# Optimization experiments

Measured on AMD Instinct MI355X. Metric: run time of the kernel, lower is better.

The kernel has to match this reference:

```python
import jax, jax.numpy as jnp
import numpy as np
from functools import partial

N_NODES = 50000
BN_EPS = 1e-5


def _renumber(src, dst, mask, n_nodes):
    # Faithful to extract_batch_edge_idx: kept edges are relabeled by the rank of
    # their node id among the sorted unique node ids APPEARING in kept edges.
    m = mask.astype(jnp.int32)
    appear = jnp.zeros(n_nodes, jnp.int32)
    appear = appear.at[src].max(m)
    appear = appear.at[dst].max(m)
    new_id = jnp.cumsum(appear) - 1  # rank of each appearing node id
    s = jnp.where(mask, new_id[src], 0)
    d = jnp.where(mask, new_id[dst], 0)
    return s, d


def _gcn_conv(x, W, b, src, dst, ew, n):
    # PyG GCNConv: linear, add self-loops, symmetric normalization, scatter-add.
    xw = x @ W                                   # [n, out]
    deg = jax.ops.segment_sum(ew, dst, num_segments=n) + 1.0  # +1 self loop
    dinv = jax.lax.rsqrt(deg)
    norm = dinv[src] * dinv[dst] * ew            # masked edges -> 0 weight
    agg = jax.ops.segment_sum(norm[:, None] * xw[src], dst, num_segments=n)
    agg = agg + (dinv * dinv)[:, None] * xw      # self-loop contribution
    return agg + b


def setup_inputs() -> dict:
    key = jax.random.key(0)
    ks = jax.random.split(key, 8)
    R, N, E, B = 3, N_NODES, 1000000, 2048
    inp, hid, out = 256, 512, 256
    features = jax.random.normal(ks[0], (R, N, inp), jnp.float32)
    W1 = jax.random.normal(ks[1], (inp, hid), jnp.float32) * (1.0 / np.sqrt(inp))
    b1 = jnp.zeros((hid,), jnp.float32)
    W2 = jax.random.normal(ks[2], (hid, out), jnp.float32) * (1.0 / np.sqrt(hid))
    b2 = jnp.zeros((out,), jnp.float32)
    gamma = jnp.ones((hid,), jnp.float32)
    beta = jnp.zeros((hid,), jnp.float32)
    edge_index = jax.random.randint(ks[3], (R, 2, E), 0, N, jnp.int64)
    # distinct, sorted batch node ids (torch code iterates node values)
    batch_nodes = jnp.sort(jax.random.permutation(ks[4], N)[:B]).astype(jnp.int64)
    return {"features": features, "W1": W1, "b1": b1, "W2": W2, "b2": b2,
            "gamma": gamma, "beta": beta, "edge_index": edge_index,
            "batch_nodes": batch_nodes}


def reference(features, W1, b1, W2, b2, gamma, beta, edge_index, batch_nodes):
    R, N, _ = features.shape
    B = batch_nodes.shape[0]
    in_batch = jnp.zeros(N, bool).at[batch_nodes].set(True)
    outs = []
    for r in range(R):  # small fixed relation count
        src, dst = edge_index[r, 0], edge_index[r, 1]
        mask = in_batch[src] & in_batch[dst]
        ew = mask.astype(features.dtype)
        s, d = _renumber(src, dst, mask, N)
        x = features[r, batch_nodes]             # [B, inp]
        h = _gcn_conv(x, W1, b1, s, d, ew, B)    # [B, hid]
        # BatchNorm1d (training mode: biased batch stats)
        mu = h.mean(axis=0)
        var = h.var(axis=0)
        h = (h - mu) * jax.lax.rsqrt(var + BN_EPS) * gamma + beta
        outs.append(_gcn_conv(h, W2, b2, s, d, ew, B))  # [B, out]
    stacked = jnp.stack(outs, axis=0)            # [R, B, out]
    return stacked.reshape(B, -1)                # row-major reshape, as torch
```

## Files before the change

### kernel.cpp

```cpp
#include <hip/hip_runtime.h>
#include <hip/hip_bf16.h>
#include <stdint.h>
#include <stddef.h>

#define RNUM   3
#define NNODES 50000
#define ENUM   1000000
#define BATCH  2048
#define INP    256
#define HID    512
#define OUTC   256
#define BN_EPS 1e-5f

typedef __bf16 bf16x8 __attribute__((ext_vector_type(8)));
typedef float  f32x4  __attribute__((ext_vector_type(4)));

__device__ inline unsigned short f2bf(float f) {
    union { float f; unsigned u; } c; c.f = f;
    unsigned u = c.u;
    return (unsigned short)((u + 0x7fffu + ((u >> 16) & 1u)) >> 16);
}

__device__ inline uint4 pack8(float4 a, float4 b) {
    uint4 r;
    r.x = (unsigned)f2bf(a.x) | ((unsigned)f2bf(a.y) << 16);
    r.y = (unsigned)f2bf(a.z) | ((unsigned)f2bf(a.w) << 16);
    r.z = (unsigned)f2bf(b.x) | ((unsigned)f2bf(b.y) << 16);
    r.w = (unsigned)f2bf(b.z) | ((unsigned)f2bf(b.w) << 16);
    return r;
}

__global__ __launch_bounds__(256) void k_wt(const float* __restrict__ W1,
                                            const float* __restrict__ W2,
                                            unsigned short* __restrict__ W1T,
                                            unsigned short* __restrict__ W2T) {
    __shared__ float T[32][33];
    int z = blockIdx.z;
    const float* W = z ? W2 : W1;
    unsigned short* WT = z ? W2T : W1T;
    int K = z ? HID : INP;
    int N = z ? OUTC : HID;
    int kt = blockIdx.y, nt = blockIdx.x;
    if (kt * 32 >= K || nt * 32 >= N) return;
    int tx = threadIdx.x & 31, ty = threadIdx.x >> 5;
#pragma unroll
    for (int j = 0; j < 4; ++j)
        T[ty + j * 8][tx] = W[(size_t)(kt * 32 + ty + j * 8) * N + nt * 32 + tx];
    __syncthreads();
#pragma unroll
    for (int j = 0; j < 4; ++j)
        WT[(size_t)(nt * 32 + ty + j * 8) * K + kt * 32 + tx] = f2bf(T[tx][ty + j * 8]);
}

__global__ void k_init(int* __restrict__ inv, int* __restrict__ appear,
                       float* __restrict__ deg, float* __restrict__ musum,
                       float* __restrict__ sqsum, int* __restrict__ kcount) {
    int i = blockIdx.x * blockDim.x + threadIdx.x;
    if (i < NNODES) inv[i] = -1;
    if (i < RNUM * BATCH) { appear[i] = 0; deg[i] = 0.0f; }
    if (i < RNUM * HID)   { musum[i] = 0.0f; sqsum[i] = 0.0f; }
    if (i < RNUM)         kcount[i] = 0;
}

__global__ void k_scatter_inv(const int* __restrict__ bn, int* __restrict__ inv) {
    int i = blockIdx.x * blockDim.x + threadIdx.x;
    if (i < BATCH) inv[bn[i]] = i;
}

__global__ void k_mask(const int* __restrict__ edge_index, const int* __restrict__ inv,
                       int* __restrict__ appear, int2* __restrict__ edges,
                       int* __restrict__ kcount) {
    int z = blockIdx.z;
    const int* src = edge_index + (size_t)z * 2 * ENUM;
    const int* dst = src + ENUM;
    int2* ed = edges + (size_t)z * ENUM;
    int* app = appear + z * BATCH;
    int stride = gridDim.x * blockDim.x;
    for (int e4 = blockIdx.x * blockDim.x + threadIdx.x; e4 < ENUM / 4; e4 += stride) {
        int4 s4 = ((const int4*)src)[e4];
        int4 d4 = ((const int4*)dst)[e4];
        int ss[4] = {s4.x, s4.y, s4.z, s4.w};
        int dd[4] = {d4.x, d4.y, d4.z, d4.w};
#pragma unroll
        for (int i = 0; i < 4; ++i) {
            int ps = inv[ss[i]];
            int pd = inv[dd[i]];
            if (ps >= 0 && pd >= 0) {
                int idx = atomicAdd(kcount + z, 1);
                ed[idx] = make_int2(ps, pd);
                app[ps] = 1;
                app[pd] = 1;
            }
        }
    }
}

__global__ __launch_bounds__(1024) void k_scan2048(const int* __restrict__ appear,
                                                   int* __restrict__ rankArr) {
    __shared__ int buf[2][BATCH];
    int z = blockIdx.x;
    const int* ap = appear + z * BATCH;
    int* rk = rankArr + z * BATCH;
    int t = threadIdx.x;
    buf[0][t] = ap[t];
    buf[0][t + 1024] = ap[t + 1024];
    __syncthreads();
    int cur = 0;
    for (int off = 1; off < BATCH; off <<= 1) {
        int nxt = cur ^ 1;
        int i1 = t, i2 = t + 1024;
        buf[nxt][i1] = buf[cur][i1] + (i1 >= off ? buf[cur][i1 - off] : 0);
        buf[nxt][i2] = buf[cur][i2] + (i2 >= off ? buf[cur][i2 - off] : 0);
        __syncthreads();
        cur = nxt;
    }
    rk[t] = buf[cur][t] - 1;
    rk[t + 1024] = buf[cur][t + 1024] - 1;
}

__global__ void k_deg(int2* __restrict__ edges, const int* __restrict__ rankArr,
                      const int* __restrict__ kcount, float* __restrict__ deg) {
    int z = blockIdx.z;
    int K = kcount[z];
    int2* ed = edges + (size_t)z * ENUM;
    const int* rk = rankArr + z * BATCH;
    float* dg = deg + z * BATCH;
    int stride = gridDim.x * blockDim.x;
    for (int e = blockIdx.x * blockDim.x + threadIdx.x; e < K; e += stride) {
        int2 E = ed[e];
        int s = rk[E.x], d = rk[E.y];
        ed[e] = make_int2(s, d);
        atomicAdd(&dg[d], 1.0f);
    }
}


__global__ __launch_bounds__(256) void k_gemm1(
    const float* __restrict__ features, const int* __restrict__ bn,
    const unsigned short* __restrict__ W1T, const float* __restrict__ b1,
    const float* __restrict__ deg, float* __restrict__ xw, float* __restrict__ hbase) {
    __shared__ __align__(16) unsigned short As[64][40];
    __shared__ __align__(16) unsigned short Bs[64][40];
    int z = blockIdx.z;
    const float* feat = features + (size_t)z * NNODES * INP;
    const float* dgz = deg + z * BATCH;
    float* xwz = xw + (size_t)z * BATCH * HID;
    float* hbz = hbase + (size_t)z * BATCH * HID;
    int m0 = blockIdx.y * 64, n0 = blockIdx.x * 64;
    int t = threadIdx.x;
    int ar = t >> 2, aq = t & 3;
    int grow = bn[m0 + ar];
    const float* aptr = feat + (size_t)grow * INP + aq * 8;
    const unsigned short* bptr = W1T + (size_t)(n0 + ar) * INP + aq * 8;

    int lane = t & 63, wave = t >> 6;
    int wm = (wave & 1) * 32, wn = (wave >> 1) * 32;
    int ml = lane & 15, quad = lane >> 4, q8 = quad * 8;

    f32x4 acc[2][2] = {};
    for (int k0 = 0; k0 < INP; k0 += 32) {
        float4 a0 = *(const float4*)(aptr + k0);
        float4 a1 = *(const float4*)(aptr + k0 + 4);
        uint4 bv = *(const uint4*)(bptr + k0);
        *(uint4*)&As[ar][aq * 8] = pack8(a0, a1);
        *(uint4*)&Bs[ar][aq * 8] = bv;
        __syncthreads();
        bf16x8 af[2], bfr[2];
#pragma unroll
        for (int mi = 0; mi < 2; ++mi) af[mi]  = *(const bf16x8*)&As[wm + mi * 16 + ml][q8];
#pragma unroll
        for (int ni = 0; ni < 2; ++ni) bfr[ni] = *(const bf16x8*)&Bs[wn + ni * 16 + ml][q8];
#pragma unroll
        for (int mi = 0; mi < 2; ++mi)
#pragma unroll
            for (int ni = 0; ni < 2; ++ni)
                acc[mi][ni] = __builtin_amdgcn_mfma_f32_16x16x32_bf16(af[mi], bfr[ni], acc[mi][ni], 0, 0, 0);
        __syncthreads();
    }
#pragma unroll
    for (int mi = 0; mi < 2; ++mi)
#pragma unroll
        for (int r = 0; r < 4; ++r) {
            int row = m0 + wm + mi * 16 + quad * 4 + r;
            float d2 = 1.0f / (dgz[row] + 1.0f);
#pragma unroll
            for (int ni = 0; ni < 2; ++ni) {
                int col = n0 + wn + ni * 16 + ml;
                float c = acc[mi][ni][r];
                xwz[(size_t)row * HID + col] = c;
                hbz[(size_t)row * HID + col] = d2 * c + b1[col];
            }
        }
}

__global__ __launch_bounds__(256) void k_gemm2(
    const float* __restrict__ hbase, const float* __restrict__ rstdg,
    const float* __restrict__ shiftc, const unsigned short* __restrict__ W2T,
    const float* __restrict__ b2, const float* __restrict__ deg,
    float* __restrict__ yw, float* __restrict__ out) {
    __shared__ __align__(16) unsigned short As[64][40];
    __shared__ __align__(16) unsigned short Bs[64][40];
    int z = blockIdx.z;
    const float* hz = hbase + (size_t)z * BATCH * HID;
    const float* gz = rstdg + z * HID;
    const float* sz = shiftc + z * HID;
    const float* dgz = deg + z * BATCH;
    float* ywz = yw + (size_t)z * BATCH * OUTC;
    float* oz = out + (size_t)z * BATCH * OUTC;
    int m0 = blockIdx.y * 64, n0 = blockIdx.x * 64;
    int t = threadIdx.x;
    int ar = t >> 2, aq = t & 3;
    const float* aptr = hz + (size_t)(m0 + ar) * HID + aq * 8;
    const unsigned short* bptr = W2T + (size_t)(n0 + ar) * HID + aq * 8;

    int lane = t & 63, wave = t >> 6;
    int wm = (wave & 1) * 32, wn = (wave >> 1) * 32;
    int ml = lane & 15, quad = lane >> 4, q8 = quad * 8;

    f32x4 acc[2][2] = {};
    for (int k0 = 0; k0 < HID; k0 += 32) {
        float4 h0 = *(const float4*)(aptr + k0);
        float4 h1 = *(const float4*)(aptr + k0 + 4);
        float4 g0 = *(const float4*)(gz + k0 + aq * 8);
        float4 g1 = *(const float4*)(gz + k0 + aq * 8 + 4);
        float4 s0 = *(const float4*)(sz + k0 + aq * 8);
        float4 s1 = *(const float4*)(sz + k0 + aq * 8 + 4);
        float4 a0 = make_float4(h0.x * g0.x + s0.x, h0.y * g0.y + s0.y,
                                h0.z * g0.z + s0.z, h0.w * g0.w + s0.w);
        float4 a1 = make_float4(h1.x * g1.x + s1.x, h1.y * g1.y + s1.y,
                                h1.z * g1.z + s1.z, h1.w * g1.w + s1.w);
        uint4 bv = *(const uint4*)(bptr + k0);
        *(uint4*)&As[ar][aq * 8] = pack8(a0, a1);
        *(uint4*)&Bs[ar][aq * 8] = bv;
        __syncthreads();
        bf16x8 af[2], bfr[2];
#pragma unroll
        for (int mi = 0; mi < 2; ++mi) af[mi]  = *(const bf16x8*)&As[wm + mi * 16 + ml][q8];
#pragma unroll
        for (int ni = 0; ni < 2; ++ni) bfr[ni] = *(const bf16x8*)&Bs[wn + ni * 16 + ml][q8];
#pragma unroll
        for (int mi = 0; mi < 2; ++mi)
#pragma unroll
            for (int ni = 0; ni < 2; ++ni)
                acc[mi][ni] = __builtin_amdgcn_mfma_f32_16x16x32_bf16(af[mi], bfr[ni], acc[mi][ni], 0, 0, 0);
        __syncthreads();
    }
#pragma unroll
    for (int mi = 0; mi < 2; ++mi)
#pragma unroll
        for (int r = 0; r < 4; ++r) {
            int row = m0 + wm + mi * 16 + quad * 4 + r;
            float d2 = 1.0f / (dgz[row] + 1.0f);
#pragma unroll
            for (int ni = 0; ni < 2; ++ni) {
                int col = n0 + wn + ni * 16 + ml;
                float c = acc[mi][ni][r];
                ywz[(size_t)row * OUTC + col] = c;
                oz[(size_t)row * OUTC + col] = d2 * c + b2[col];
            }
        }
}

__global__ void k_agg(const int2* __restrict__ edges, const int* __restrict__ kcount,
                      const float* __restrict__ deg, const float* __restrict__ src_mat,
                      float* __restrict__ dst_mat, int ncol) {
    int z = blockIdx.z;
    int K = kcount[z];
    const int2* ed = edges + (size_t)z * ENUM;
    const float* dgz = deg + z * BATCH;
    const float* sm = src_mat + (size_t)z * BATCH * ncol;
    float* dm = dst_mat + (size_t)z * BATCH * ncol;
    for (int e = blockIdx.x; e < K; e += gridDim.x) {
        int2 E = ed[e];
        float w = rsqrtf(dgz[E.x] + 1.0f) * rsqrtf(dgz[E.y] + 1.0f);
        const float* srow = sm + (size_t)E.x * ncol;
        float* drow = dm + (size_t)E.y * ncol;
        for (int c = threadIdx.x; c < ncol; c += blockDim.x)
            atomicAdd(&drow[c], w * srow[c]);
    }
}

__global__ __launch_bounds__(256) void k_bnstats(const float* __restrict__ hbase,
                                                 float* __restrict__ musum,
                                                 float* __restrict__ sqsum) {
    int z = blockIdx.z;
    const float* h = hbase + (size_t)z * BATCH * HID;
    int c0 = threadIdx.x;
    int r0 = blockIdx.x * 32;
    float s1a = 0, s2a = 0, s1b = 0, s2b = 0;
    for (int rr = 0; rr < 32; ++rr) {
        const float* row = h + (size_t)(r0 + rr) * HID;
        float va = row[c0];
        float vb = row[c0 + 256];
        s1a += va; s2a += va * va;
        s1b += vb; s2b += vb * vb;
    }
    atomicAdd(&musum[z * HID + c0], s1a);       atomicAdd(&sqsum[z * HID + c0], s2a);
    atomicAdd(&musum[z * HID + c0 + 256], s1b); atomicAdd(&sqsum[z * HID + c0 + 256], s2b);
}

__global__ void k_bnfinal(const float* __restrict__ musum, const float* __restrict__ sqsum,
                          const float* __restrict__ gamma, const float* __restrict__ beta,
                          float* __restrict__ rstdg, float* __restrict__ shiftc) {
    int z = blockIdx.x;
    int c = threadIdx.x;
    float mu = musum[z * HID + c] * (1.0f / BATCH);
    float ex2 = sqsum[z * HID + c] * (1.0f / BATCH);
    float var = ex2 - mu * mu;
    float g = rsqrtf(var + BN_EPS) * gamma[c];
    rstdg[z * HID + c] = g;
    shiftc[z * HID + c] = beta[c] - mu * g;
}

extern "C" void kernel_launch(void* const* d_in, const int* in_sizes, int n_in,
                              void* d_out, int out_size, void* d_ws, size_t ws_size,
                              hipStream_t stream) {
    const float* features    = (const float*)d_in[0];
    const float* W1          = (const float*)d_in[1];
    const float* b1          = (const float*)d_in[2];
    const float* W2          = (const float*)d_in[3];
    const float* b2          = (const float*)d_in[4];
    const float* gamma       = (const float*)d_in[5];
    const float* beta        = (const float*)d_in[6];
    const int*   edge_index  = (const int*)d_in[7];
    const int*   batch_nodes = (const int*)d_in[8];
    float* out = (float*)d_out;

    char* p = (char*)d_ws;
    size_t cur = 0;
    auto alloc = [&](size_t bytes) {
        void* r = p + cur;
        cur = (cur + bytes + 255) & ~(size_t)255;
        return r;
    };
    int*   inv    = (int*)  alloc(NNODES * sizeof(int));
    int*   appear = (int*)  alloc(RNUM * BATCH * sizeof(int));
    int*   rankA  = (int*)  alloc(RNUM * BATCH * sizeof(int));
    int*   kcount = (int*)  alloc(RNUM * sizeof(int));
    float* deg    = (float*)alloc(RNUM * BATCH * sizeof(float));
    float* musum  = (float*)alloc(RNUM * HID * sizeof(float));
    float* sqsum  = (float*)alloc(RNUM * HID * sizeof(float));
    float* rstdg  = (float*)alloc(RNUM * HID * sizeof(float));
    float* shiftc = (float*)alloc(RNUM * HID * sizeof(float));
    unsigned short* W1T = (unsigned short*)alloc((size_t)HID * INP * sizeof(unsigned short));
    unsigned short* W2T = (unsigned short*)alloc((size_t)OUTC * HID * sizeof(unsigned short));
    int2*  edges  = (int2*) alloc((size_t)RNUM * ENUM * sizeof(int2));
    float* xw     = (float*)alloc((size_t)RNUM * BATCH * HID * sizeof(float));
    float* hbase  = (float*)alloc((size_t)RNUM * BATCH * HID * sizeof(float));
    float* yw     = (float*)alloc((size_t)RNUM * BATCH * OUTC * sizeof(float));
    (void)ws_size; (void)in_sizes; (void)n_in; (void)out_size;

    k_wt<<<dim3(16, 16, 2), 256, 0, stream>>>(W1, W2, W1T, W2T);
    k_init<<<(NNODES + 255) / 256, 256, 0, stream>>>(inv, appear, deg, musum, sqsum, kcount);
    k_scatter_inv<<<BATCH / 256, 256, 0, stream>>>(batch_nodes, inv);

    k_mask<<<dim3(512, 1, RNUM), 256, 0, stream>>>(edge_index, inv, appear, edges, kcount);
    k_scan2048<<<RNUM, 1024, 0, stream>>>(appear, rankA);
    k_deg<<<dim3(64, 1, RNUM), 256, 0, stream>>>(edges, rankA, kcount, deg);

    k_gemm1<<<dim3(HID / 64, BATCH / 64, RNUM), 256, 0, stream>>>(
        features, batch_nodes, W1T, b1, deg, xw, hbase);
    k_agg<<<dim3(256, 1, RNUM), 256, 0, stream>>>(edges, kcount, deg, xw, hbase, HID);

    k_bnstats<<<dim3(64, 1, RNUM), 256, 0, stream>>>(hbase, musum, sqsum);
    k_bnfinal<<<RNUM, HID, 0, stream>>>(musum, sqsum, gamma, beta, rstdg, shiftc);

    k_gemm2<<<dim3(OUTC / 64, BATCH / 64, RNUM), 256, 0, stream>>>(
        hbase, rstdg, shiftc, W2T, b2, deg, yw, out);
    k_agg<<<dim3(256, 1, RNUM), 256, 0, stream>>>(edges, kcount, deg, yw, out, OUTC);
}
```

Before: 328.1 us.

## Fuse setup, mask+GEMM1, scan+degree and BN-finalize into fewer kernel launches

Merges the init, weight-transpose and bf16 feature gather into one setup kernel, and fuses edge masking (now a shared-memory bitmap membership test) with the first GEMM in a single grid. It also replaces the 2048-wide scan and degree kernels with one wave-shuffle scan plus shared-memory degree accumulation per relation. The BN finalize step is folded into GEMM2, and the h computation moves into the BN stats kernel via a separate aggregation buffer. This cuts the launch count and the repeated fp32 feature conversion. In exchange it adds an extra buffer pass and serializes each relation's degree counting within a single block.

After: 322.6 us, median of 2. No clear change (-1.7%).

```diff
diff --git a/kernel.cpp b/kernel.cpp
--- a/kernel.cpp
+++ b/kernel.cpp
@@ -11,6 +11,9 @@
 #define HID    512
 #define OUTC   256
 #define BN_EPS 1e-5f
+#define NBLK   768
+#define NTHR   256
+#define BMW    1568
 
 typedef __bf16 bf16x8 __attribute__((ext_vector_type(8)));
 typedef float  f32x4  __attribute__((ext_vector_type(4)));
@@ -30,235 +33,200 @@
     return r;
 }
 
-__global__ __launch_bounds__(256) void k_wt(const float* __restrict__ W1,
-                                            const float* __restrict__ W2,
-                                            unsigned short* __restrict__ W1T,
-                                            unsigned short* __restrict__ W2T) {
-    __shared__ float T[32][33];
-    int z = blockIdx.z;
-    const float* W = z ? W2 : W1;
-    unsigned short* WT = z ? W2T : W1T;
-    int K = z ? HID : INP;
-    int N = z ? OUTC : HID;
-    int kt = blockIdx.y, nt = blockIdx.x;
-    if (kt * 32 >= K || nt * 32 >= N) return;
-    int tx = threadIdx.x & 31, ty = threadIdx.x >> 5;
-#pragma unroll
-    for (int j = 0; j < 4; ++j)
-        T[ty + j * 8][tx] = W[(size_t)(kt * 32 + ty + j * 8) * N + nt * 32 + tx];
-    __syncthreads();
-#pragma unroll
-    for (int j = 0; j < 4; ++j)
-        WT[(size_t)(nt * 32 + ty + j * 8) * K + kt * 32 + tx] = f2bf(T[tx][ty + j * 8]);
-}
-
-__global__ void k_init(int* __restrict__ inv, int* __restrict__ appear,
-                       float* __restrict__ deg, float* __restrict__ musum,
-                       float* __restrict__ sqsum, int* __restrict__ kcount) {
-    int i = blockIdx.x * blockDim.x + threadIdx.x;
-    if (i < NNODES) inv[i] = -1;
-    if (i < RNUM * BATCH) { appear[i] = 0; deg[i] = 0.0f; }
-    if (i < RNUM * HID)   { musum[i] = 0.0f; sqsum[i] = 0.0f; }
-    if (i < RNUM)         kcount[i] = 0;
-}
-
-__global__ void k_scatter_inv(const int* __restrict__ bn, int* __restrict__ inv) {
-    int i = blockIdx.x * blockDim.x + threadIdx.x;
-    if (i < BATCH) inv[bn[i]] = i;
-}
-
-__global__ void k_mask(const int* __restrict__ edge_index, const int* __restrict__ inv,
-                       int* __restrict__ appear, int2* __restrict__ edges,
-                       int* __restrict__ kcount) {
-    int z = blockIdx.z;
-    const int* src = edge_index + (size_t)z * 2 * ENUM;
-    const int* dst = src + ENUM;
-    int2* ed = edges + (size_t)z * ENUM;
-    int* app = appear + z * BATCH;
-    int stride = gridDim.x * blockDim.x;
-    for (int e4 = blockIdx.x * blockDim.x + threadIdx.x; e4 < ENUM / 4; e4 += stride) {
-        int4 s4 = ((const int4*)src)[e4];
-        int4 d4 = ((const int4*)dst)[e4];
-        int ss[4] = {s4.x, s4.y, s4.z, s4.w};
-        int dd[4] = {d4.x, d4.y, d4.z, d4.w};
-#pragma unroll
-        for (int i = 0; i < 4; ++i) {
-            int ps = inv[ss[i]];
-            int pd = inv[dd[i]];
-            if (ps >= 0 && pd >= 0) {
-                int idx = atomicAdd(kcount + z, 1);
-                ed[idx] = make_int2(ps, pd);
-                app[ps] = 1;
-                app[pd] = 1;
+__global__ __launch_bounds__(256) void k_setup(
+    const float* __restrict__ features, const float* __restrict__ W1,
+    const float* __restrict__ W2, const int* __restrict__ bn,
+    unsigned* __restrict__ bitmap, int* __restrict__ inv,
+    int* __restrict__ appear, int* __restrict__ kcount,
+    float* __restrict__ musum, float* __restrict__ sqsum,
+    float* __restrict__ aggbuf,
+    unsigned short* __restrict__ W1T, unsigned short* __restrict__ W2T,
+    unsigned short* __restrict__ featB) {
+    __shared__ float T[32 * 33];
+    const int tid = threadIdx.x;
+    const int bid = blockIdx.x;
+
+    {
+        float4* a4 = (float4*)aggbuf;
+        int base = bid * 1024;
+#pragma unroll
+        for (int j = 0; j < 4; ++j)
+            a4[base + j * 256 + tid] = make_float4(0.f, 0.f, 0.f, 0.f);
+    }
+
+    if (bid == 0) {
+        for (int i = tid; i < BMW; i += NTHR) bitmap[i] = 0u;
+        __syncthreads();
+        for (int i = tid; i < BATCH; i += NTHR) {
+            int v = bn[i];
+            atomicOr(&bitmap[v >> 5], 1u << (v & 31));
+        }
+    } else if (bid == 1) {
+        for (int i = tid; i < BATCH; i += NTHR) inv[bn[i]] = i;
+        for (int i = tid; i < RNUM * BATCH; i += NTHR) appear[i] = 0;
+        for (int i = tid; i < RNUM * HID; i += NTHR) { musum[i] = 0.f; sqsum[i] = 0.f; }
+        if (tid < RNUM) kcount[tid] = 0;
+    }
+
+    if (bid < 256) {
+        int i = bid;
+        int z = i >> 7; i &= 127;
+        const float* W = z ? W2 : W1;
+        unsigned short* WT = z ? W2T : W1T;
+        int K = z ? HID : INP;
+        int N = z ? OUTC : HID;
+        int kt, nt;
+        if (z == 0) { nt = i & 15; kt = i >> 4; } else { nt = i & 7; kt = i >> 3; }
+        int tx = tid & 31, ty = tid >> 5;
+#pragma unroll
+        for (int j = 0; j < 4; ++j)
+            T[(ty + j * 8) * 33 + tx] = W[(size_t)(kt * 32 + ty + j * 8) * N + nt * 32 + tx];
+        __syncthreads();
+#pragma unroll
+        for (int j = 0; j < 4; ++j)
+            WT[(size_t)(nt * 32 + ty + j * 8) * K + kt * 32 + tx] = f2bf(T[tx * 33 + ty + j * 8]);
+    } else if (bid < 640) {
+        int i = bid - 256;
+        int row = i * 16 + (tid >> 4);
+        int c0 = (tid & 15) * 16;
+        int z = row >> 11, m = row & 2047;
+        const float* srow = features + ((size_t)z * NNODES + bn[m]) * INP;
+        unsigned short* drow = featB + (size_t)row * INP;
+        float4 f0 = *(const float4*)(srow + c0);
+        float4 f1 = *(const float4*)(srow + c0 + 4);
+        float4 f2 = *(const float4*)(srow + c0 + 8);
+        float4 f3 = *(const float4*)(srow + c0 + 12);
+        *(uint4*)(drow + c0)     = pack8(f0, f1);
+        *(uint4*)(drow + c0 + 8) = pack8(f2, f3);
+    }
+}
+
+__global__ __launch_bounds__(256) void k_maskgemm1(
+    const int* __restrict__ edge_index, const unsigned* __restrict__ bitmap,
+    const int* __restrict__ inv, int* __restrict__ appear,
+    int* __restrict__ kcount, int2* __restrict__ edges,
+    const unsigned short* __restrict__ featB,
+    const unsigned short* __restrict__ W1T, float* __restrict__ xw) {
+    __shared__ __align__(16) unsigned char smem[10240];
+    const int tid = threadIdx.x;
+    const int bid = blockIdx.x;
+
+    {
+        unsigned* bmL = (unsigned*)smem;
+        for (int i = tid; i < BMW; i += NTHR) bmL[i] = bitmap[i];
+        __syncthreads();
+        const int gsz = NBLK * NTHR;
+        const int g0 = bid * NTHR + tid;
+        for (int z = 0; z < RNUM; ++z) {
+            const int4* s4 = (const int4*)(edge_index + (size_t)z * 2 * ENUM);
+            const int4* d4 = (const int4*)(edge_index + (size_t)z * 2 * ENUM + ENUM);
+            int2* ed = edges + (size_t)z * ENUM;
+            int* app = appear + z * BATCH;
+            for (int i = g0; i < ENUM / 4; i += gsz) {
+                int4 S = s4[i], D = d4[i];
+                int ss[4] = {S.x, S.y, S.z, S.w};
+                int dd[4] = {D.x, D.y, D.z, D.w};
+#pragma unroll
+                for (int u = 0; u < 4; ++u) {
+                    int s = ss[u], d = dd[u];
+                    unsigned ks = (bmL[s >> 5] >> (s & 31)) & 1u;
+                    unsigned kd = (bmL[d >> 5] >> (d & 31)) & 1u;
+                    if (ks & kd) {
+                        int ps = inv[s], pd = inv[d];
+                        int idx = atomicAdd(&kcount[z], 1);
+                        ed[idx] = make_int2(ps, pd);
+                        app[ps] = 1;
+                        app[pd] = 1;
+                    }
+                }
             }
         }
-    }
-}
-
-__global__ __launch_bounds__(1024) void k_scan2048(const int* __restrict__ appear,
-                                                   int* __restrict__ rankArr) {
-    __shared__ int buf[2][BATCH];
-    int z = blockIdx.x;
+        __syncthreads();
+    }
+
+    {
+        unsigned short* As = (unsigned short*)smem;
+        unsigned short* Bs = (unsigned short*)(smem + 5120);
+        int z = bid >> 8;
+        int r = bid & 255;
+        int n0 = (r & 7) * 64, m0 = (r >> 3) * 64;
+        int ar = tid >> 2, aq = tid & 3;
+        const unsigned short* aptr = featB + (size_t)(z * BATCH + m0 + ar) * INP + aq * 8;
+        const unsigned short* bptr = W1T + (size_t)(n0 + ar) * INP + aq * 8;
+        int lane = tid & 63, wave = tid >> 6;
+        int wm = (wave & 1) * 32, wn = (wave >> 1) * 32;
+        int ml = lane & 15, quad = lane >> 4, q8 = quad * 8;
+        f32x4 acc[2][2] = {};
+        for (int k0 = 0; k0 < INP; k0 += 32) {
+            uint4 av = *(const uint4*)(aptr + k0);
+            uint4 bv = *(const uint4*)(bptr + k0);
+            *(uint4*)&As[ar * 40 + aq * 8] = av;
+            *(uint4*)&Bs[ar * 40 + aq * 8] = bv;
+            __syncthreads();
+            bf16x8 af[2], bfr[2];
+#pragma unroll
+            for (int mi = 0; mi < 2; ++mi) af[mi]  = *(const bf16x8*)&As[(wm + mi * 16 + ml) * 40 + q8];
+#pragma unroll
+            for (int ni = 0; ni < 2; ++ni) bfr[ni] = *(const bf16x8*)&Bs[(wn + ni * 16 + ml) * 40 + q8];
+#pragma unroll
+            for (int mi = 0; mi < 2; ++mi)
+#pragma unroll
+                for (int ni = 0; ni < 2; ++ni)
+                    acc[mi][ni] = __builtin_amdgcn_mfma_f32_16x16x32_bf16(af[mi], bfr[ni], acc[mi][ni], 0, 0, 0);
+            __syncthreads();
+        }
+        float* xwz = xw + (size_t)z * BATCH * HID;
+#pragma unroll
+        for (int mi = 0; mi < 2; ++mi)
+#pragma unroll
+            for (int rr = 0; rr < 4; ++rr) {
+                int row = m0 + wm + mi * 16 + quad * 4 + rr;
+#pragma unroll
+                for (int ni = 0; ni < 2; ++ni) {
+                    int col = n0 + wn + ni * 16 + ml;
+                    xwz[(size_t)row * HID + col] = acc[mi][ni][rr];
+                }
+            }
+    }
+}
+
+__global__ __launch_bounds__(256) void k_scandeg(
+    const int* __restrict__ appear, const int* __restrict__ kcount,
+    int2* __restrict__ edges, float* __restrict__ deg) {
+    __shared__ int rk[BATCH];
+    __shared__ float dgf[BATCH];
+    __shared__ int wsums[4];
+    const int tid = threadIdx.x;
+    const int z = blockIdx.x;
     const int* ap = appear + z * BATCH;
-    int* rk = rankArr + z * BATCH;
-    int t = threadIdx.x;
-    buf[0][t] = ap[t];
-    buf[0][t + 1024] = ap[t + 1024];
+    int b0 = tid * 8;
+    int pre[8]; int run = 0;
+#pragma unroll
+    for (int j = 0; j < 8; ++j) { run += ap[b0 + j]; pre[j] = run; }
+    int lane = tid & 63, wv = tid >> 6;
+    int sc = run;
+    for (int off = 1; off < 64; off <<= 1) {
+        int n = __shfl_up(sc, off);
+        if (lane >= off) sc += n;
+    }
+    if (lane == 63) wsums[wv] = sc;
     __syncthreads();
-    int cur = 0;
-    for (int off = 1; off < BATCH; off <<= 1) {
-        int nxt = cur ^ 1;
-        int i1 = t, i2 = t + 1024;
-        buf[nxt][i1] = buf[cur][i1] + (i1 >= off ? buf[cur][i1 - off] : 0);
-        buf[nxt][i2] = buf[cur][i2] + (i2 >= off ? buf[cur][i2 - off] : 0);
-        __syncthreads();
-        cur = nxt;
-    }
-    rk[t] = buf[cur][t] - 1;
-    rk[t + 1024] = buf[cur][t + 1024] - 1;
-}
-
-__global__ void k_deg(int2* __restrict__ edges, const int* __restrict__ rankArr,
-                      const int* __restrict__ kcount, float* __restrict__ deg) {
-    int z = blockIdx.z;
+    int base = sc - run;
+    for (int w = 0; w < wv; ++w) base += wsums[w];
+#pragma unroll
+    for (int j = 0; j < 8; ++j) { rk[b0 + j] = base + pre[j] - 1; dgf[b0 + j] = 0.f; }
+    __syncthreads();
     int K = kcount[z];
     int2* ed = edges + (size_t)z * ENUM;
-    const int* rk = rankArr + z * BATCH;
-    float* dg = deg + z * BATCH;
-    int stride = gridDim.x * blockDim.x;
-    for (int e = blockIdx.x * blockDim.x + threadIdx.x; e < K; e += stride) {
+    for (int e = tid; e < K; e += NTHR) {
         int2 E = ed[e];
         int s = rk[E.x], d = rk[E.y];
         ed[e] = make_int2(s, d);
-        atomicAdd(&dg[d], 1.0f);
-    }
-}
-
-
-__global__ __launch_bounds__(256) void k_gemm1(
-    const float* __restrict__ features, const int* __restrict__ bn,
-    const unsigned short* __restrict__ W1T, const float* __restrict__ b1,
-    const float* __restrict__ deg, float* __restrict__ xw, float* __restrict__ hbase) {
-    __shared__ __align__(16) unsigned short As[64][40];
-    __shared__ __align__(16) unsigned short Bs[64][40];
-    int z = blockIdx.z;
-    const float* feat = features + (size_t)z * NNODES * INP;
-    const float* dgz = deg + z * BATCH;
-    float* xwz = xw + (size_t)z * BATCH * HID;
-    float* hbz = hbase + (size_t)z * BATCH * HID;
-    int m0 = blockIdx.y * 64, n0 = blockIdx.x * 64;
-    int t = threadIdx.x;
-    int ar = t >> 2, aq = t & 3;
-    int grow = bn[m0 + ar];
-    const float* aptr = feat + (size_t)grow * INP + aq * 8;
-    const unsigned short* bptr = W1T + (size_t)(n0 + ar) * INP + aq * 8;
-
-    int lane = t & 63, wave = t >> 6;
-    int wm = (wave & 1) * 32, wn = (wave >> 1) * 32;
-    int ml = lane & 15, quad = lane >> 4, q8 = quad * 8;
-
-    f32x4 acc[2][2] = {};
-    for (int k0 = 0; k0 < INP; k0 += 32) {
-        float4 a0 = *(const float4*)(aptr + k0);
-        float4 a1 = *(const float4*)(aptr + k0 + 4);
-        uint4 bv = *(const uint4*)(bptr + k0);
-        *(uint4*)&As[ar][aq * 8] = pack8(a0, a1);
-        *(uint4*)&Bs[ar][aq * 8] = bv;
-        __syncthreads();
-        bf16x8 af[2], bfr[2];
-#pragma unroll
-        for (int mi = 0; mi < 2; ++mi) af[mi]  = *(const bf16x8*)&As[wm + mi * 16 + ml][q8];
-#pragma unroll
-        for (int ni = 0; ni < 2; ++ni) bfr[ni] = *(const bf16x8*)&Bs[wn + ni * 16 + ml][q8];
-#pragma unroll
-        for (int mi = 0; mi < 2; ++mi)
-#pragma unroll
-            for (int ni = 0; ni < 2; ++ni)
-                acc[mi][ni] = __builtin_amdgcn_mfma_f32_16x16x32_bf16(af[mi], bfr[ni], acc[mi][ni], 0, 0, 0);
-        __syncthreads();
-    }
-#pragma unroll
-    for (int mi = 0; mi < 2; ++mi)
-#pragma unroll
-        for (int r = 0; r < 4; ++r) {
-            int row = m0 + wm + mi * 16 + quad * 4 + r;
-            float d2 = 1.0f / (dgz[row] + 1.0f);
-#pragma unroll
-            for (int ni = 0; ni < 2; ++ni) {
-                int col = n0 + wn + ni * 16 + ml;
-                float c = acc[mi][ni][r];
-                xwz[(size_t)row * HID + col] = c;
-                hbz[(size_t)row * HID + col] = d2 * c + b1[col];
-            }
-        }
-}
-
-__global__ __launch_bounds__(256) void k_gemm2(
-    const float* __restrict__ hbase, const float* __restrict__ rstdg,
-    const float* __restrict__ shiftc, const unsigned short* __restrict__ W2T,
-    const float* __restrict__ b2, const float* __restrict__ deg,
-    float* __restrict__ yw, float* __restrict__ out) {
-    __shared__ __align__(16) unsigned short As[64][40];
-    __shared__ __align__(16) unsigned short Bs[64][40];
-    int z = blockIdx.z;
-    const float* hz = hbase + (size_t)z * BATCH * HID;
-    const float* gz = rstdg + z * HID;
-    const float* sz = shiftc + z * HID;
-    const float* dgz = deg + z * BATCH;
-    float* ywz = yw + (size_t)z * BATCH * OUTC;
-    float* oz = out + (size_t)z * BATCH * OUTC;
-    int m0 = blockIdx.y * 64, n0 = blockIdx.x * 64;
-    int t = threadIdx.x;
-    int ar = t >> 2, aq = t & 3;
-    const float* aptr = hz + (size_t)(m0 + ar) * HID + aq * 8;
-    const unsigned short* bptr = W2T + (size_t)(n0 + ar) * HID + aq * 8;
-
-    int lane = t & 63, wave = t >> 6;
-    int wm = (wave & 1) * 32, wn = (wave >> 1) * 32;
-    int ml = lane & 15, quad = lane >> 4, q8 = quad * 8;
-
-    f32x4 acc[2][2] = {};
-    for (int k0 = 0; k0 < HID; k0 += 32) {
-        float4 h0 = *(const float4*)(aptr + k0);
-        float4 h1 = *(const float4*)(aptr + k0 + 4);
-        float4 g0 = *(const float4*)(gz + k0 + aq * 8);
-        float4 g1 = *(const float4*)(gz + k0 + aq * 8 + 4);
-        float4 s0 = *(const float4*)(sz + k0 + aq * 8);
-        float4 s1 = *(const float4*)(sz + k0 + aq * 8 + 4);
-        float4 a0 = make_float4(h0.x * g0.x + s0.x, h0.y * g0.y + s0.y,
-                                h0.z * g0.z + s0.z, h0.w * g0.w + s0.w);
-        float4 a1 = make_float4(h1.x * g1.x + s1.x, h1.y * g1.y + s1.y,
-                                h1.z * g1.z + s1.z, h1.w * g1.w + s1.w);
-        uint4 bv = *(const uint4*)(bptr + k0);
-        *(uint4*)&As[ar][aq * 8] = pack8(a0, a1);
-        *(uint4*)&Bs[ar][aq * 8] = bv;
-        __syncthreads();
-        bf16x8 af[2], bfr[2];
-#pragma unroll
-        for (int mi = 0; mi < 2; ++mi) af[mi]  = *(const bf16x8*)&As[wm + mi * 16 + ml][q8];
-#pragma unroll
-        for (int ni = 0; ni < 2; ++ni) bfr[ni] = *(const bf16x8*)&Bs[wn + ni * 16 + ml][q8];
-#pragma unroll
-        for (int mi = 0; mi < 2; ++mi)
-#pragma unroll
-            for (int ni = 0; ni < 2; ++ni)
-                acc[mi][ni] = __builtin_amdgcn_mfma_f32_16x16x32_bf16(af[mi], bfr[ni], acc[mi][ni], 0, 0, 0);
-        __syncthreads();
-    }
-#pragma unroll
-    for (int mi = 0; mi < 2; ++mi)
-#pragma unroll
-        for (int r = 0; r < 4; ++r) {
-            int row = m0 + wm + mi * 16 + quad * 4 + r;
-            float d2 = 1.0f / (dgz[row] + 1.0f);
-#pragma unroll
-            for (int ni = 0; ni < 2; ++ni) {
-                int col = n0 + wn + ni * 16 + ml;
-                float c = acc[mi][ni][r];
-                ywz[(size_t)row * OUTC + col] = c;
-                oz[(size_t)row * OUTC + col] = d2 * c + b2[col];
-            }
-        }
+        atomicAdd(&dgf[d], 1.0f);
+    }
+    __syncthreads();
+    float* dz = deg + z * BATCH;
+    for (int i = tid; i < BATCH; i += NTHR) dz[i] = dgf[i];
 }
 
 __global__ void k_agg(const int2* __restrict__ edges, const int* __restrict__ kcount,
@@ -280,36 +248,108 @@
     }
 }
 
-__global__ __launch_bounds__(256) void k_bnstats(const float* __restrict__ hbase,
-                                                 float* __restrict__ musum,
-                                                 float* __restrict__ sqsum) {
+__global__ __launch_bounds__(256) void k_hbn(
+    const float* __restrict__ xw, const float* __restrict__ aggbuf,
+    const float* __restrict__ deg, const float* __restrict__ b1,
+    float* __restrict__ hbase, float* __restrict__ musum,
+    float* __restrict__ sqsum) {
     int z = blockIdx.z;
-    const float* h = hbase + (size_t)z * BATCH * HID;
+    const float* xz = xw + (size_t)z * BATCH * HID;
+    const float* az = aggbuf + (size_t)z * BATCH * HID;
+    float* hz = hbase + (size_t)z * BATCH * HID;
+    const float* dgz = deg + z * BATCH;
     int c0 = threadIdx.x;
     int r0 = blockIdx.x * 32;
+    float b1a = b1[c0], b1b = b1[c0 + 256];
     float s1a = 0, s2a = 0, s1b = 0, s2b = 0;
     for (int rr = 0; rr < 32; ++rr) {
-        const float* row = h + (size_t)(r0 + rr) * HID;
-        float va = row[c0];
-        float vb = row[c0 + 256];
-        s1a += va; s2a += va * va;
-        s1b += vb; s2b += vb * vb;
+        int row = r0 + rr;
+        float d2 = 1.0f / (dgz[row] + 1.0f);
+        size_t off = (size_t)row * HID + c0;
+        float ha = xz[off] * d2 + b1a + az[off];
+        float hb = xz[off + 256] * d2 + b1b + az[off + 256];
+        hz[off] = ha;
+        hz[off + 256] = hb;
+        s1a += ha; s2a += ha * ha;
+        s1b += hb; s2b += hb * hb;
     }
     atomicAdd(&musum[z * HID + c0], s1a);       atomicAdd(&sqsum[z * HID + c0], s2a);
     atomicAdd(&musum[z * HID + c0 + 256], s1b); atomicAdd(&sqsum[z * HID + c0 + 256], s2b);
 }
 
-__global__ void k_bnfinal(const float* __restrict__ musum, const float* __restrict__ sqsum,
-                          const float* __restrict__ gamma, const float* __restrict__ beta,
-                          float* __restrict__ rstdg, float* __restrict__ shiftc) {
-    int z = blockIdx.x;
-    int c = threadIdx.x;
-    float mu = musum[z * HID + c] * (1.0f / BATCH);
-    float ex2 = sqsum[z * HID + c] * (1.0f / BATCH);
-    float var = ex2 - mu * mu;
-    float g = rsqrtf(var + BN_EPS) * gamma[c];
-    rstdg[z * HID + c] = g;
-    shiftc[z * HID + c] = beta[c] - mu * g;
+__global__ __launch_bounds__(256) void k_gemm2f(
+    const float* __restrict__ hbase, const float* __restrict__ musum,
+    const float* __restrict__ sqsum, const float* __restrict__ gamma,
+    const float* __restrict__ beta, const unsigned short* __restrict__ W2T,
+    const float* __restrict__ b2, const float* __restrict__ deg,
+    float* __restrict__ yw, float* __restrict__ out) {
+    __shared__ __align__(16) unsigned short As[64][40];
+    __shared__ __align__(16) unsigned short Bs[64][40];
+    __shared__ float gL[HID];
+    __shared__ float sL[HID];
+    int z = blockIdx.z;
+    int m0 = blockIdx.y * 64, n0 = blockIdx.x * 64;
+    int tid = threadIdx.x;
+    for (int c = tid; c < HID; c += NTHR) {
+        float mu  = musum[z * HID + c] * (1.0f / BATCH);
+        float ex2 = sqsum[z * HID + c] * (1.0f / BATCH);
+        float var = ex2 - mu * mu;
+        float g = rsqrtf(var + BN_EPS) * gamma[c];
+        gL[c] = g;
+        sL[c] = beta[c] - mu * g;
+    }
+    __syncthreads();
+    int ar = tid >> 2, aq = tid & 3;
+    const float* aptr = hbase + (size_t)z * BATCH * HID + (size_t)(m0 + ar) * HID + aq * 8;
+    const unsigned short* bptr = W2T + (size_t)(n0 + ar) * HID + aq * 8;
+    int lane = tid & 63, wave = tid >> 6;
+    int wm = (wave & 1) * 32, wn = (wave >> 1) * 32;
+    int ml = lane & 15, quad = lane >> 4, q8 = quad * 8;
+    f32x4 acc[2][2] = {};
+    for (int k0 = 0; k0 < HID; k0 += 32) {
+        float4 h0 = *(const float4*)(aptr + k0);
+        float4 h1 = *(const float4*)(aptr + k0 + 4);
+        float4 g0 = *(const float4*)(gL + k0 + aq * 8);
+        float4 g1 = *(const float4*)(gL + k0 + aq * 8 + 4);
+        float4 s0 = *(const float4*)(sL + k0 + aq * 8);
+        float4 s1 = *(const float4*)(sL + k0 + aq * 8 + 4);
+        float4 a0 = make_float4(h0.x * g0.x + s0.x, h0.y * g0.y + s0.y,
+                                h0.z * g0.z + s0.z, h0.w * g0.w + s0.w);
+        float4 a1 = make_float4(h1.x * g1.x + s1.x, h1.y * g1.y + s1.y,
+                                h1.z * g1.z + s1.z, h1.w * g1.w + s1.w);
+        uint4 bv = *(const uint4*)(bptr + k0);
+        *(uint4*)&As[ar][aq * 8] = pack8(a0, a1);
+        *(uint4*)&Bs[ar][aq * 8] = bv;
+        __syncthreads();
+        bf16x8 af[2], bfr[2];
+#pragma unroll
+        for (int mi = 0; mi < 2; ++mi) af[mi]  = *(const bf16x8*)&As[wm + mi * 16 + ml][q8];
+#pragma unroll
+        for (int ni = 0; ni < 2; ++ni) bfr[ni] = *(const bf16x8*)&Bs[wn + ni * 16 + ml][q8];
+#pragma unroll
+        for (int mi = 0; mi < 2; ++mi)
+#pragma unroll
+            for (int ni = 0; ni < 2; ++ni)
+                acc[mi][ni] = __builtin_amdgcn_mfma_f32_16x16x32_bf16(af[mi], bfr[ni], acc[mi][ni], 0, 0, 0);
+        __syncthreads();
+    }
+    const float* dgz = deg + z * BATCH;
+    float* ywz = yw + (size_t)z * BATCH * OUTC;
+    float* oz = out + (size_t)z * BATCH * OUTC;
+#pragma unroll
+    for (int mi = 0; mi < 2; ++mi)
+#pragma unroll
+        for (int rr = 0; rr < 4; ++rr) {
+            int row = m0 + wm + mi * 16 + quad * 4 + rr;
+            float d2 = 1.0f / (dgz[row] + 1.0f);
+#pragma unroll
+            for (int ni = 0; ni < 2; ++ni) {
+                int col = n0 + wn + ni * 16 + ml;
+                float c = acc[mi][ni][rr];
+                ywz[(size_t)row * OUTC + col] = c;
+                oz[(size_t)row * OUTC + col] = d2 * c + b2[col];
+            }
+        }
 }
 
 extern "C" void kernel_launch(void* const* d_in, const int* in_sizes, int n_in,
@@ -335,37 +375,37 @@
     };
     int*   inv    = (int*)  alloc(NNODES * sizeof(int));
     int*   appear = (int*)  alloc(RNUM * BATCH * sizeof(int));
-    int*   rankA  = (int*)  alloc(RNUM * BATCH * sizeof(int));
     int*   kcount = (int*)  alloc(RNUM * sizeof(int));
     float* deg    = (float*)alloc(RNUM * BATCH * sizeof(float));
     float* musum  = (float*)alloc(RNUM * HID * sizeof(float));
     float* sqsum  = (float*)alloc(RNUM * HID * sizeof(float));
-    float* rstdg  = (float*)alloc(RNUM * HID * sizeof(float));
-    float* shiftc = (float*)alloc(RNUM * HID * sizeof(float));
+    unsigned* bitmap = (unsigned*)alloc(BMW * sizeof(unsigned));
     unsigned short* W1T = (unsigned short*)alloc((size_t)HID * INP * sizeof(unsigned short));
     unsigned short* W2T = (unsigned short*)alloc((size_t)OUTC * HID * sizeof(unsigned short));
+    unsigned short* featB = (unsigned short*)alloc((size_t)RNUM * BATCH * INP * sizeof(unsigned short));
     int2*  edges  = (int2*) alloc((size_t)RNUM * ENUM * sizeof(int2));
     float* xw     = (float*)alloc((size_t)RNUM * BATCH * HID * sizeof(float));
+    float* aggbuf = (float*)alloc((size_t)RNUM * BATCH * HID * sizeof(float));
     float* hbase  = (float*)alloc((size_t)RNUM * BATCH * HID * sizeof(float));
     float* yw     = (float*)alloc((size_t)RNUM * BATCH * OUTC * sizeof(float));
     (void)ws_size; (void)in_sizes; (void)n_in; (void)out_size;
 
-    k_wt<<<dim3(16, 16, 2), 256, 0, stream>>>(W1, W2, W1T, W2T);
-    k_init<<<(NNODES + 255) / 256, 256, 0, stream>>>(inv, appear, deg, musum, sqsum, kcount);
-    k_scatter_inv<<<BATCH / 256, 256, 0, stream>>>(batch_nodes, inv);
-
-    k_mask<<<dim3(512, 1, RNUM), 256, 0, stream>>>(edge_index, inv, appear, edges, kcount);
-    k_scan2048<<<RNUM, 1024, 0, stream>>>(appear, rankA);
-    k_deg<<<dim3(64, 1, RNUM), 256, 0, stream>>>(edges, rankA, kcount, deg);
-
-    k_gemm1<<<dim3(HID / 64, BATCH / 64, RNUM), 256, 0, stream>>>(
-        features, batch_nodes, W1T, b1, deg, xw, hbase);
-    k_agg<<<dim3(256, 1, RNUM), 256, 0, stream>>>(edges, kcount, deg, xw, hbase, HID);
-
-    k_bnstats<<<dim3(64, 1, RNUM), 256, 0, stream>>>(hbase, musum, sqsum);
-    k_bnfinal<<<RNUM, HID, 0, stream>>>(musum, sqsum, gamma, beta, rstdg, shiftc);
-
-    k_gemm2<<<dim3(OUTC / 64, BATCH / 64, RNUM), 256, 0, stream>>>(
-        hbase, rstdg, shiftc, W2T, b2, deg, yw, out);
-    k_agg<<<dim3(256, 1, RNUM), 256, 0, stream>>>(edges, kcount, deg, yw, out, OUTC);
-}
+    k_setup<<<NBLK, NTHR, 0, stream>>>(features, W1, W2, batch_nodes,
+                                       bitmap, inv, appear, kcount,
+                                       musum, sqsum, aggbuf, W1T, W2T, featB);
+
+    k_maskgemm1<<<NBLK, NTHR, 0, stream>>>(edge_index, bitmap, inv, appear,
+                                           kcount, edges, featB, W1T, xw);
+
+    k_scandeg<<<RNUM, NTHR, 0, stream>>>(appear, kcount, edges, deg);
+
+    k_agg<<<dim3(256, 1, RNUM), NTHR, 0, stream>>>(edges, kcount, deg, xw, aggbuf, HID);
+
+    k_hbn<<<dim3(64, 1, RNUM), NTHR, 0, stream>>>(xw, aggbuf, deg, b1,
+                                                  hbase, musum, sqsum);
+
+    k_gemm2f<<<dim3(OUTC / 64, BATCH / 64, RNUM), NTHR, 0, stream>>>(
+        hbase, musum, sqsum, gamma, beta, W2T, b2, deg, yw, out);
+
+    k_agg<<<dim3(256, 1, RNUM), NTHR, 0, stream>>>(edges, kcount, deg, yw, out, OUTC);
+}
```
